# Kernel optimization log

Measured on AMD Instinct MI355X. Metric: run time of the kernel, lower is better.

## Reference

```python
import jax, jax.numpy as jnp
import numpy as np

D_MODEL, N_LEVELS, N_HEADS, N_POINTS = 256, 4, 8, 4
SHAPES = [(100, 100), (50, 50), (25, 25), (13, 13)]  # (H, W) per level


def setup_inputs() -> dict:
    key = jax.random.key(0)
    ks = jax.random.split(key, 8)
    N = 2
    C = D_MODEL
    Len_in = sum(h * w for h, w in SHAPES)
    Lq = Len_in  # encoder self-attention
    query = jax.random.normal(ks[0], (N, Lq, C), jnp.float32)
    reference_points = jax.random.uniform(ks[1], (N, Lq, N_LEVELS, 2), dtype=jnp.float32)
    input_flatten = jax.random.normal(ks[2], (N, Len_in, C), jnp.float32)
    input_spatial_shapes = np.array(SHAPES, dtype=np.int64)
    areas = input_spatial_shapes[:, 0] * input_spatial_shapes[:, 1]
    input_level_start_index = np.concatenate([[0], np.cumsum(areas)[:-1]]).astype(np.int64)
    s = 1.0 / np.sqrt(C)
    Wv = jax.random.uniform(ks[3], (C, C), jnp.float32, -s, s)
    bv = jnp.zeros((C,), jnp.float32)
    # sampling_offsets: small random weight + the module's grid bias init
    Woff = jax.random.normal(ks[4], (N_HEADS * N_LEVELS * N_POINTS * 2, C), jnp.float32) * 0.01
    thetas = jnp.arange(N_HEADS, dtype=jnp.float32) * (2.0 * np.pi / N_HEADS)
    grid = jnp.stack([jnp.cos(thetas), jnp.sin(thetas)], -1)  # (M,2)
    grid = grid / jnp.max(jnp.abs(grid), axis=-1, keepdims=True)
    grid = jnp.tile(grid[:, None, None, :], (1, N_LEVELS, N_POINTS, 1))
    grid = grid * (jnp.arange(N_POINTS, dtype=jnp.float32) + 1.0)[None, None, :, None]
    boff = grid.reshape(-1)
    Wa = jax.random.normal(ks[5], (N_HEADS * N_LEVELS * N_POINTS, C), jnp.float32) * 0.02
    ba = jnp.zeros((N_HEADS * N_LEVELS * N_POINTS,), jnp.float32)
    Wo = jax.random.uniform(ks[6], (C, C), jnp.float32, -s, s)
    bo = jnp.zeros((C,), jnp.float32)
    return {
        'query': query, 'reference_points': reference_points, 'input_flatten': input_flatten,
        'input_spatial_shapes': input_spatial_shapes, 'input_level_start_index': input_level_start_index,
        'Wv': Wv, 'bv': bv, 'Woff': Woff, 'boff': boff, 'Wa': Wa, 'ba': ba, 'Wo': Wo, 'bo': bo,
    }


def _msda_forward(query, reference_points, input_flatten, shapes, starts,
                  Wv, bv, Woff, boff, Wa, ba, Wo, bo):
    N, Lq, C = query.shape
    M, L, P = N_HEADS, N_LEVELS, N_POINTS
    D = C // M
    value = (input_flatten @ Wv.T + bv).reshape(N, -1, M, D)  # (N, Len_in, M, D)
    off = (query @ Woff.T + boff).reshape(N, Lq, M, L, P, 2)
    attn = jax.nn.softmax((query @ Wa.T + ba).reshape(N, Lq, M, L * P), axis=-1)
    attn = attn.reshape(N, Lq, M, L, P)
    # offset_normalizer = (W_l, H_l)
    norm = jnp.asarray(shapes[:, ::-1].copy(), jnp.float32)  # (L, 2)
    loc = reference_points[:, :, None, :, None, :] + off / norm[None, None, None, :, None, :]
    grids = 2.0 * loc - 1.0  # (N, Lq, M, L, P, 2), grid_sample convention
    out = jnp.zeros((N, Lq, M, D), query.dtype)
    for l in range(L):
        H, W = int(shapes[l, 0]), int(shapes[l, 1])
        s0 = int(starts[l])
        v = value[:, s0:s0 + H * W]  # (N, H*W, M, D)
        # align_corners=False unnormalization
        gx = ((grids[:, :, :, l, :, 0] + 1.0) * W - 1.0) / 2.0  # (N, Lq, M, P)
        gy = ((grids[:, :, :, l, :, 1] + 1.0) * H - 1.0) / 2.0
        x0 = jnp.floor(gx); y0 = jnp.floor(gy)
        fx = gx - x0;       fy = gy - y0
        x0i = x0.astype(jnp.int32); y0i = y0.astype(jnp.int32)

        def gather(iy, ix):
            valid = (iy >= 0) & (iy < H) & (ix >= 0) & (ix < W)
            lin = jnp.clip(iy, 0, H - 1) * W + jnp.clip(ix, 0, W - 1)  # (N, Lq, M, P)
            lin2 = lin.transpose(0, 1, 3, 2).reshape(N, Lq * P, M)
            g = jnp.take_along_axis(v, lin2[..., None], axis=1)  # (N, Lq*P, M, D)
            g = g.reshape(N, Lq, P, M, D).transpose(0, 1, 3, 2, 4)  # (N, Lq, M, P, D)
            return g * valid[..., None]  # zero padding outside

        s00 = gather(y0i, x0i)
        s01 = gather(y0i, x0i + 1)
        s10 = gather(y0i + 1, x0i)
        s11 = gather(y0i + 1, x0i + 1)
        sampled = (s00 * ((1 - fy) * (1 - fx))[..., None] + s01 * ((1 - fy) * fx)[..., None]
                   + s10 * (fy * (1 - fx))[..., None] + s11 * (fy * fx)[..., None])
        out = out + jnp.einsum('nqmp,nqmpd->nqmd', attn[:, :, :, l], sampled)
    out = out.reshape(N, Lq, C)
    return out @ Wo.T + bo


def reference(query, reference_points, input_flatten, input_spatial_shapes, input_level_start_index,
              Wv, bv, Woff, boff, Wa, ba, Wo, bo):
    shapes = np.asarray(input_spatial_shapes)
    starts = np.asarray(input_level_start_index)
    return _msda_forward(query, reference_points, input_flatten, shapes, starts,
                         Wv, bv, Woff, boff, Wa, ba, Wo, bo)
```

## Files before the change

kernel.cpp:

```cpp
#include <hip/hip_runtime.h>
#include <math.h>

#define NB   2
#define LQ   13294
#define NROWS (NB*LQ)
#define CDIM 256

typedef unsigned short u16;
typedef unsigned int   u32;
typedef short bf16x8 __attribute__((ext_vector_type(8)));
typedef float f32x4  __attribute__((ext_vector_type(4)));

struct alignas(8) U16x4 { u16 x, y, z, w; };

__device__ __forceinline__ u16 f2bf(float f) {
    u32 u = __builtin_bit_cast(u32, f);
    u += 0x7FFFu + ((u >> 16) & 1u);
    return (u16)(u >> 16);
}
__device__ __forceinline__ float bf2f(u16 h) {
    u32 u = ((u32)h) << 16;
    return __builtin_bit_cast(float, u);
}

__device__ __forceinline__ void gload_lds16(const void* g, void* l) {
    __builtin_amdgcn_global_load_lds(
        (__attribute__((address_space(1))) void*)g,
        (__attribute__((address_space(3))) void*)l, 16, 0, 0);
}

__global__ __launch_bounds__(256)
void prep_all(const float4* __restrict__ query, const float4* __restrict__ inflat,
              const float* __restrict__ Wv, const float* __restrict__ Woff,
              const float* __restrict__ Wa, const float* __restrict__ Wo,
              const float* __restrict__ boff, const float* __restrict__ ba,
              u16* __restrict__ qb, u16* __restrict__ ib,
              u16* __restrict__ wb, float* __restrict__ biascat) {
    const int b = blockIdx.x;
    const int t = threadIdx.x;
    if (b < 6647) {
        int i = b * 256 + t;
        float4 v = query[i];
        U16x4 o{f2bf(v.x), f2bf(v.y), f2bf(v.z), f2bf(v.w)};
        *(U16x4*)&qb[(size_t)i * 4] = o;
    } else if (b < 13294) {
        int i = (b - 6647) * 256 + t;
        float4 v = inflat[i];
        U16x4 o{f2bf(v.x), f2bf(v.y), f2bf(v.z), f2bf(v.w)};
        *(U16x4*)&ib[(size_t)i * 4] = o;
    } else {
        int i = (b - 13294) * 256 + t;
        float v;
        if      (i <  65536) v = Wv[i];
        else if (i < 131072) v = Woff[i - 65536];
        else if (i < 163840) v = Wa[i - 131072];
        else                 v = Wo[i - 163840];
        wb[i] = f2bf(v);
        if (b == 13294) {
            biascat[t] = boff[t];
            if (t < 128) biascat[256 + t] = ba[t];
        }
    }
}

__device__ __forceinline__ void gemm_core128(
    const u16* __restrict__ A, const u16* __restrict__ Bw, int M, int row0,
    u16* As, u16* Bs, f32x4 (&acc)[4][4]) {
    const int tid  = threadIdx.x;
    const int lane = tid & 63;
    const int wave = tid >> 6;
    const int ln16 = lane & 15;
    const int kq   = lane >> 4;
    const int wr   = (wave >> 1) * 64;
    const int wc   = (wave & 1) * 64;

    #pragma unroll
    for (int kt = 0; kt < 4; ++kt) {
        const int k0 = kt * 64;
        #pragma unroll
        for (int it = 0; it < 4; ++it) {
            int chunk = it * 256 + tid;
            int row = chunk >> 3;
            int ch  = chunk & 7;
            int chs = (ch ^ (row & 7)) * 8;
            int gra = min(row0 + row, M - 1);
            gload_lds16(A  + (size_t)gra * 256 + k0 + chs, As + chunk * 8);
            gload_lds16(Bw + (size_t)row * 256 + k0 + chs, Bs + chunk * 8);
        }
        __syncthreads();
        #pragma unroll
        for (int kf = 0; kf < 2; ++kf) {
            const int ck = kf * 4 + kq;
            bf16x8 a[4], b[4];
            #pragma unroll
            for (int i = 0; i < 4; ++i) {
                int r = wr + i * 16 + ln16;
                a[i] = *(const bf16x8*)&As[r * 64 + ((ck ^ (r & 7)) * 8)];
                int c = wc + i * 16 + ln16;
                b[i] = *(const bf16x8*)&Bs[c * 64 + ((ck ^ (c & 7)) * 8)];
            }
            #pragma unroll
            for (int i = 0; i < 4; ++i)
                #pragma unroll
                for (int j = 0; j < 4; ++j)
                    acc[i][j] = __builtin_amdgcn_mfma_f32_16x16x32_bf16(
                        a[i], b[j], acc[i][j], 0, 0, 0);
        }
        __syncthreads();
    }
}

__global__ __launch_bounds__(256, 3)
void gemm_front(const u16* __restrict__ qb, const u16* __restrict__ ib,
                const u16* __restrict__ wb, const float* __restrict__ bv,
                const float* __restrict__ bcat, u16* __restrict__ value,
                float* __restrict__ offb, float* __restrict__ logit, int M) {
    __shared__ u16 As[128 * 64];
    __shared__ u16 Bs[128 * 64];
    const int s    = blockIdx.x;
    const int row0 = blockIdx.y * 128;
    const u16* A  = (s < 2) ? ib : qb;
    const u16* Bw = wb + (size_t)s * 32768;
    const float* bias = (s < 2) ? bv + s * 128 : bcat + (s - 2) * 128;

    f32x4 acc[4][4] = {};
    gemm_core128(A, Bw, M, row0, As, Bs, acc);

    const int lane = threadIdx.x & 63;
    const int wave = threadIdx.x >> 6;
    const int ln16 = lane & 15, kq = lane >> 4;
    const int wr = (wave >> 1) * 64, wc = (wave & 1) * 64;
    #pragma unroll
    for (int j = 0; j < 4; ++j) {
        int lc = wc + j * 16 + ln16;
        float bj = bias[lc];
        #pragma unroll
        for (int i = 0; i < 4; ++i) {
            #pragma unroll
            for (int r = 0; r < 4; ++r) {
                int gr = row0 + wr + i * 16 + kq * 4 + r;
                if (gr < M) {
                    float o = acc[i][j][r] + bj;
                    if (s < 2)
                        value[(size_t)gr * 256 + s * 128 + lc] = f2bf(o);
                    else if (s < 4)
                        offb[(size_t)gr * 256 + (s - 2) * 128 + lc] = o;
                    else
                        logit[(size_t)gr * 128 + lc] = o;
                }
            }
        }
    }
}

__global__ __launch_bounds__(256, 3)
void gemm_out(const u16* __restrict__ A, const u16* __restrict__ Bw0,
              const float* __restrict__ bias, float* __restrict__ C, int M) {
    __shared__ u16 As[128 * 64];
    __shared__ u16 Bs[128 * 64];
    const int s    = blockIdx.x;
    const int row0 = blockIdx.y * 128;
    const u16* Bw = Bw0 + (size_t)s * 32768;

    f32x4 acc[4][4] = {};
    gemm_core128(A, Bw, M, row0, As, Bs, acc);

    const int lane = threadIdx.x & 63;
    const int wave = threadIdx.x >> 6;
    const int ln16 = lane & 15, kq = lane >> 4;
    const int wr = (wave >> 1) * 64, wc = (wave & 1) * 64;
    #pragma unroll
    for (int j = 0; j < 4; ++j) {
        int gc = s * 128 + wc + j * 16 + ln16;
        float bj = bias[gc];
        #pragma unroll
        for (int i = 0; i < 4; ++i) {
            #pragma unroll
            for (int r = 0; r < 4; ++r) {
                int gr = row0 + wr + i * 16 + kq * 4 + r;
                if (gr < M) C[(size_t)gr * 256 + gc] = acc[i][j][r] + bj;
            }
        }
    }
}

__global__ __launch_bounds__(256)
void msda_sample(const u16* __restrict__ value,
                 const float* __restrict__ refpts,
                 const float* __restrict__ off,
                 const float* __restrict__ logits,
                 u16* __restrict__ tmp) {
    __shared__ float sAw[4][8][16];
    __shared__ int   sLin[4][8][17][4];
    __shared__ float sW[4][8][17][4];

    const int t  = threadIdx.x;
    const int qb = blockIdx.x * 4;

    if (t < 32) {
        const int qi = t >> 3, m = t & 7;
        const float* lg = logits + (size_t)(qb + qi) * 128 + m * 16;
        float e[16];
        float mx = -1e30f;
        #pragma unroll
        for (int i = 0; i < 16; ++i) { e[i] = lg[i]; mx = fmaxf(mx, e[i]); }
        float s = 0.f;
        #pragma unroll
        for (int i = 0; i < 16; ++i) { e[i] = __expf(e[i] - mx); s += e[i]; }
        const float inv = 1.f / s;
        #pragma unroll
        for (int i = 0; i < 16; ++i) sAw[qi][m][i] = e[i] * inv;
    }
    __syncthreads();

    #pragma unroll
    for (int j2 = 0; j2 < 2; ++j2) {
        const int job = t + j2 * 256;
        const int qi = job >> 7;
        const int m  = (job >> 4) & 7;
        const int p  = job & 15;
        const int l  = p >> 2, pp = p & 3;
        const int q  = qb + qi;
        const int n  = (q >= LQ) ? 1 : 0;

        const int W = (l == 0) ? 100 : (l == 1) ? 50 : (l == 2) ? 25 : 13;
        const int H = W;
        const int st = (l == 0) ? 0 : (l == 1) ? 10000 : (l == 2) ? 12500 : 13125;

        const float rx = refpts[(size_t)q * 8 + l * 2 + 0];
        const float ry = refpts[(size_t)q * 8 + l * 2 + 1];
        const float ox = off[(size_t)q * 256 + m * 32 + (l * 4 + pp) * 2 + 0];
        const float oy = off[(size_t)q * 256 + m * 32 + (l * 4 + pp) * 2 + 1];

        const float locx = rx + ox / (float)W;
        const float locy = ry + oy / (float)H;
        const float grx = 2.f * locx - 1.f;
        const float gry = 2.f * locy - 1.f;
        const float gx = ((grx + 1.f) * (float)W - 1.f) * 0.5f;
        const float gy = ((gry + 1.f) * (float)H - 1.f) * 0.5f;
        const float x0f = floorf(gx), y0f = floorf(gy);
        const float fx = gx - x0f, fy = gy - y0f;
        const int x0 = (int)x0f, y0 = (int)y0f;
        const int x1 = x0 + 1, y1 = y0 + 1;

        const int cx0 = min(max(x0, 0), W - 1);
        const int cx1 = min(max(x1, 0), W - 1);
        const int cy0 = min(max(y0, 0), H - 1);
        const int cy1 = min(max(y1, 0), H - 1);
        const bool vx0 = (x0 >= 0) & (x0 < W);
        const bool vx1 = (x1 >= 0) & (x1 < W);
        const bool vy0 = (y0 >= 0) & (y0 < H);
        const bool vy1 = (y1 >= 0) & (y1 < H);

        const float aw = sAw[qi][m][p];
        const int base = n * LQ + st;
        sLin[qi][m][p][0] = base + cy0 * W + cx0;
        sLin[qi][m][p][1] = base + cy0 * W + cx1;
        sLin[qi][m][p][2] = base + cy1 * W + cx0;
        sLin[qi][m][p][3] = base + cy1 * W + cx1;
        sW[qi][m][p][0] = (vy0 & vx0) ? aw * (1.f - fy) * (1.f - fx) : 0.f;
        sW[qi][m][p][1] = (vy0 & vx1) ? aw * (1.f - fy) * fx         : 0.f;
        sW[qi][m][p][2] = (vy1 & vx0) ? aw * fy * (1.f - fx)         : 0.f;
        sW[qi][m][p][3] = (vy1 & vx1) ? aw * fy * fx                 : 0.f;
    }
    __syncthreads();

    const int qi = t >> 6;
    const int m  = (t >> 3) & 7;
    const int e  = t & 7;
    const int q  = qb + qi;
    const u16* vch = value + m * 32 + e * 4;

    float ax = 0.f, ay = 0.f, az = 0.f, aw_ = 0.f;
    #pragma unroll
    for (int g = 0; g < 4; ++g) {
        U16x4 raw[16];
        float4 Wt4[4];
        #pragma unroll
        for (int pp = 0; pp < 4; ++pp) {
            int p = g * 4 + pp;
            int4 L = *(const int4*)&sLin[qi][m][p][0];
            Wt4[pp] = *(const float4*)&sW[qi][m][p][0];
            raw[pp * 4 + 0] = *(const U16x4*)(vch + (size_t)L.x * 256);
            raw[pp * 4 + 1] = *(const U16x4*)(vch + (size_t)L.y * 256);
            raw[pp * 4 + 2] = *(const U16x4*)(vch + (size_t)L.z * 256);
            raw[pp * 4 + 3] = *(const U16x4*)(vch + (size_t)L.w * 256);
        }
        #pragma unroll
        for (int pp = 0; pp < 4; ++pp) {
            const float* wp = (const float*)&Wt4[pp];
            #pragma unroll
            for (int c = 0; c < 4; ++c) {
                U16x4 r = raw[pp * 4 + c];
                float wgt = wp[c];
                ax  += wgt * bf2f(r.x);
                ay  += wgt * bf2f(r.y);
                az  += wgt * bf2f(r.z);
                aw_ += wgt * bf2f(r.w);
            }
        }
    }
    U16x4 o{f2bf(ax), f2bf(ay), f2bf(az), f2bf(aw_)};
    *(U16x4*)&tmp[(size_t)q * 256 + m * 32 + e * 4] = o;
}

extern "C" void kernel_launch(void* const* d_in, const int* in_sizes, int n_in,
                              void* d_out, int out_size, void* d_ws, size_t ws_size,
                              hipStream_t stream) {
    const float* query  = (const float*)d_in[0];
    const float* refpts = (const float*)d_in[1];
    const float* inflat = (const float*)d_in[2];
    const float* Wv   = (const float*)d_in[5];
    const float* bv   = (const float*)d_in[6];
    const float* Woff = (const float*)d_in[7];
    const float* boff = (const float*)d_in[8];
    const float* Wa   = (const float*)d_in[9];
    const float* ba   = (const float*)d_in[10];
    const float* Wo   = (const float*)d_in[11];
    const float* bo   = (const float*)d_in[12];
    float* out = (float*)d_out;

    char* ws = (char*)d_ws;
    constexpr size_t SZ16 = (size_t)NROWS * 256 * 2;
    constexpr size_t SZ32 = (size_t)NROWS * 256 * 4;
    constexpr size_t SZL  = (size_t)NROWS * 128 * 4;
    u16*   qb    = (u16*)(ws);
    u16*   ib    = (u16*)(ws + SZ16);
    u16*   value = (u16*)(ws + 2 * SZ16);
    float* offb  = (float*)(ws + 3 * SZ16);
    float* logit = (float*)(ws + 3 * SZ16 + SZ32);
    u16*   wb    = (u16*)(ws + 3 * SZ16 + SZ32 + SZL);
    float* bcat  = (float*)(ws + 3 * SZ16 + SZ32 + SZL + 229376 * 2);
    u16*   tmp   = qb;

    const int RG = (NROWS + 127) / 128;

    hipLaunchKernelGGL(prep_all, dim3(14190), dim3(256), 0, stream,
                       (const float4*)query, (const float4*)inflat,
                       Wv, Woff, Wa, Wo, boff, ba, qb, ib, wb, bcat);

    gemm_front<<<dim3(5, RG), dim3(256), 0, stream>>>(
        qb, ib, wb, bv, bcat, value, offb, logit, NROWS);

    hipLaunchKernelGGL(msda_sample, dim3(NROWS / 4), dim3(256), 0, stream,
                       value, refpts, offb, logit, tmp);

    gemm_out<<<dim3(2, RG), dim3(256), 0, stream>>>(
        tmp, wb + 163840, bo, out, NROWS);
}
```

Before: 232.5 us.

## Fuse fp32-to-bf16 conversion into GEMM loads and vectorize MSDA gather

Removes the separate prep kernel that converted query, input and weights to bf16. The GEMMs now read fp32 directly, convert in registers with packed cvt instructions and store to swizzled LDS. This drops one launch and a bf16 round-trip through memory, at the cost of losing the async global-to-LDS loads for the A operand. The sampling kernel is also reworked: each thread gathers 16-byte chunks over half the points using packed f32x2 FMAs, then combines the two halves with a lane shuffle, and the division by W becomes a multiply by its reciprocal.

```diff
diff --git a/kernel.cpp b/kernel.cpp
--- a/kernel.cpp
+++ b/kernel.cpp
@@ -10,6 +10,7 @@
 typedef unsigned int   u32;
 typedef short bf16x8 __attribute__((ext_vector_type(8)));
 typedef float f32x4  __attribute__((ext_vector_type(4)));
+typedef float f32x2  __attribute__((ext_vector_type(2)));
 
 struct alignas(8) U16x4 { u16 x, y, z, w; };
 
@@ -23,48 +24,27 @@
     return __builtin_bit_cast(float, u);
 }
 
+__device__ __forceinline__ u32 cvtpk(float a, float b) {
+    u32 d;
+    asm("v_cvt_pk_bf16_f32 %0, %1, %2" : "=v"(d) : "v"(a), "v"(b));
+    return d;
+}
+
 __device__ __forceinline__ void gload_lds16(const void* g, void* l) {
     __builtin_amdgcn_global_load_lds(
         (__attribute__((address_space(1))) void*)g,
         (__attribute__((address_space(3))) void*)l, 16, 0, 0);
 }
 
-__global__ __launch_bounds__(256)
-void prep_all(const float4* __restrict__ query, const float4* __restrict__ inflat,
-              const float* __restrict__ Wv, const float* __restrict__ Woff,
-              const float* __restrict__ Wa, const float* __restrict__ Wo,
-              const float* __restrict__ boff, const float* __restrict__ ba,
-              u16* __restrict__ qb, u16* __restrict__ ib,
-              u16* __restrict__ wb, float* __restrict__ biascat) {
-    const int b = blockIdx.x;
-    const int t = threadIdx.x;
-    if (b < 6647) {
-        int i = b * 256 + t;
-        float4 v = query[i];
-        U16x4 o{f2bf(v.x), f2bf(v.y), f2bf(v.z), f2bf(v.w)};
-        *(U16x4*)&qb[(size_t)i * 4] = o;
-    } else if (b < 13294) {
-        int i = (b - 6647) * 256 + t;
-        float4 v = inflat[i];
-        U16x4 o{f2bf(v.x), f2bf(v.y), f2bf(v.z), f2bf(v.w)};
-        *(U16x4*)&ib[(size_t)i * 4] = o;
-    } else {
-        int i = (b - 13294) * 256 + t;
-        float v;
-        if      (i <  65536) v = Wv[i];
-        else if (i < 131072) v = Woff[i - 65536];
-        else if (i < 163840) v = Wa[i - 131072];
-        else                 v = Wo[i - 163840];
-        wb[i] = f2bf(v);
-        if (b == 13294) {
-            biascat[t] = boff[t];
-            if (t < 128) biascat[256 + t] = ba[t];
-        }
-    }
-}
-
-__device__ __forceinline__ void gemm_core128(
-    const u16* __restrict__ A, const u16* __restrict__ Bw, int M, int row0,
+__device__ __forceinline__ f32x2 bfpair(u32 u) {
+    union { u32 w[2]; f32x2 v; } x;
+    x.w[0] = u << 16;
+    x.w[1] = u & 0xFFFF0000u;
+    return x.v;
+}
+
+__device__ __forceinline__ void core_f32src(
+    const float* __restrict__ A, const float* __restrict__ Bf, int M, int row0,
     u16* As, u16* Bs, f32x4 (&acc)[4][4]) {
     const int tid  = threadIdx.x;
     const int lane = tid & 63;
@@ -82,10 +62,22 @@
             int chunk = it * 256 + tid;
             int row = chunk >> 3;
             int ch  = chunk & 7;
-            int chs = (ch ^ (row & 7)) * 8;
+            int dst = row * 64 + ((ch ^ (row & 7)) * 8);
             int gra = min(row0 + row, M - 1);
-            gload_lds16(A  + (size_t)gra * 256 + k0 + chs, As + chunk * 8);
-            gload_lds16(Bw + (size_t)row * 256 + k0 + chs, Bs + chunk * 8);
+            const float* pa = A + (size_t)gra * 256 + k0 + ch * 8;
+            float4 a0 = *(const float4*)pa;
+            float4 a1 = *(const float4*)(pa + 4);
+            uint4 ua;
+            ua.x = cvtpk(a0.x, a0.y); ua.y = cvtpk(a0.z, a0.w);
+            ua.z = cvtpk(a1.x, a1.y); ua.w = cvtpk(a1.z, a1.w);
+            *(uint4*)&As[dst] = ua;
+            const float* pb = Bf + (size_t)row * 256 + k0 + ch * 8;
+            float4 b0 = *(const float4*)pb;
+            float4 b1 = *(const float4*)(pb + 4);
+            uint4 ub;
+            ub.x = cvtpk(b0.x, b0.y); ub.y = cvtpk(b0.z, b0.w);
+            ub.z = cvtpk(b1.x, b1.y); ub.w = cvtpk(b1.z, b1.w);
+            *(uint4*)&Bs[dst] = ub;
         }
         __syncthreads();
         #pragma unroll
@@ -110,21 +102,82 @@
     }
 }
 
+__device__ __forceinline__ void core_mixed(
+    const u16* __restrict__ A, const float* __restrict__ Bf, int M, int row0,
+    u16* As, u16* Bs, f32x4 (&acc)[4][4]) {
+    const int tid  = threadIdx.x;
+    const int lane = tid & 63;
+    const int wave = tid >> 6;
+    const int ln16 = lane & 15;
+    const int kq   = lane >> 4;
+    const int wr   = (wave >> 1) * 64;
+    const int wc   = (wave & 1) * 64;
+
+    #pragma unroll
+    for (int kt = 0; kt < 4; ++kt) {
+        const int k0 = kt * 64;
+        #pragma unroll
+        for (int it = 0; it < 4; ++it) {
+            int chunk = it * 256 + tid;
+            int row = chunk >> 3;
+            int ch  = chunk & 7;
+            int chs = (ch ^ (row & 7)) * 8;
+            int gra = min(row0 + row, M - 1);
+            gload_lds16(A + (size_t)gra * 256 + k0 + chs, As + chunk * 8);
+            const float* pb = Bf + (size_t)row * 256 + k0 + ch * 8;
+            float4 b0 = *(const float4*)pb;
+            float4 b1 = *(const float4*)(pb + 4);
+            uint4 ub;
+            ub.x = cvtpk(b0.x, b0.y); ub.y = cvtpk(b0.z, b0.w);
+            ub.z = cvtpk(b1.x, b1.y); ub.w = cvtpk(b1.z, b1.w);
+            *(uint4*)&Bs[row * 64 + chs] = ub;
+        }
+        __syncthreads();
+        #pragma unroll
+        for (int kf = 0; kf < 2; ++kf) {
+            const int ck = kf * 4 + kq;
+            bf16x8 a[4], b[4];
+            #pragma unroll
+            for (int i = 0; i < 4; ++i) {
+                int r = wr + i * 16 + ln16;
+                a[i] = *(const bf16x8*)&As[r * 64 + ((ck ^ (r & 7)) * 8)];
+                int c = wc + i * 16 + ln16;
+                b[i] = *(const bf16x8*)&Bs[c * 64 + ((ck ^ (c & 7)) * 8)];
+            }
+            #pragma unroll
+            for (int i = 0; i < 4; ++i)
+                #pragma unroll
+                for (int j = 0; j < 4; ++j)
+                    acc[i][j] = __builtin_amdgcn_mfma_f32_16x16x32_bf16(
+                        a[i], b[j], acc[i][j], 0, 0, 0);
+        }
+        __syncthreads();
+    }
+}
+
 __global__ __launch_bounds__(256, 3)
-void gemm_front(const u16* __restrict__ qb, const u16* __restrict__ ib,
-                const u16* __restrict__ wb, const float* __restrict__ bv,
-                const float* __restrict__ bcat, u16* __restrict__ value,
-                float* __restrict__ offb, float* __restrict__ logit, int M) {
+void gemm_front(const float* __restrict__ query, const float* __restrict__ inflat,
+                const float* __restrict__ Wv, const float* __restrict__ Woff,
+                const float* __restrict__ Wa, const float* __restrict__ bv,
+                const float* __restrict__ boff, const float* __restrict__ ba,
+                u16* __restrict__ value, float* __restrict__ offb,
+                float* __restrict__ logit, int M) {
     __shared__ u16 As[128 * 64];
     __shared__ u16 Bs[128 * 64];
     const int s    = blockIdx.x;
     const int row0 = blockIdx.y * 128;
-    const u16* A  = (s < 2) ? ib : qb;
-    const u16* Bw = wb + (size_t)s * 32768;
-    const float* bias = (s < 2) ? bv + s * 128 : bcat + (s - 2) * 128;
+    const float* A  = (s < 2) ? inflat : query;
+    const float* Bf = (s == 0) ? Wv
+                    : (s == 1) ? Wv + 32768
+                    : (s == 2) ? Woff
+                    : (s == 3) ? Woff + 32768
+                    : Wa;
+    const float* bias = (s < 2) ? bv + s * 128
+                      : (s < 4) ? boff + (s - 2) * 128
+                      : ba;
 
     f32x4 acc[4][4] = {};
-    gemm_core128(A, Bw, M, row0, As, Bs, acc);
+    core_f32src(A, Bf, M, row0, As, Bs, acc);
 
     const int lane = threadIdx.x & 63;
     const int wave = threadIdx.x >> 6;
@@ -154,16 +207,16 @@
 }
 
 __global__ __launch_bounds__(256, 3)
-void gemm_out(const u16* __restrict__ A, const u16* __restrict__ Bw0,
+void gemm_out(const u16* __restrict__ A, const float* __restrict__ Wo,
               const float* __restrict__ bias, float* __restrict__ C, int M) {
     __shared__ u16 As[128 * 64];
     __shared__ u16 Bs[128 * 64];
     const int s    = blockIdx.x;
     const int row0 = blockIdx.y * 128;
-    const u16* Bw = Bw0 + (size_t)s * 32768;
+    const float* Bf = Wo + (size_t)s * 32768;
 
     f32x4 acc[4][4] = {};
-    gemm_core128(A, Bw, M, row0, As, Bs, acc);
+    core_mixed(A, Bf, M, row0, As, Bs, acc);
 
     const int lane = threadIdx.x & 63;
     const int wave = threadIdx.x >> 6;
@@ -226,14 +279,16 @@
         const int W = (l == 0) ? 100 : (l == 1) ? 50 : (l == 2) ? 25 : 13;
         const int H = W;
         const int st = (l == 0) ? 0 : (l == 1) ? 10000 : (l == 2) ? 12500 : 13125;
+        const float invW = (l == 0) ? 0.01f : (l == 1) ? 0.02f
+                         : (l == 2) ? 0.04f : (1.f / 13.f);
 
         const float rx = refpts[(size_t)q * 8 + l * 2 + 0];
         const float ry = refpts[(size_t)q * 8 + l * 2 + 1];
         const float ox = off[(size_t)q * 256 + m * 32 + (l * 4 + pp) * 2 + 0];
         const float oy = off[(size_t)q * 256 + m * 32 + (l * 4 + pp) * 2 + 1];
 
-        const float locx = rx + ox / (float)W;
-        const float locy = ry + oy / (float)H;
+        const float locx = rx + ox * invW;
+        const float locy = ry + oy * invW;
         const float grx = 2.f * locx - 1.f;
         const float gry = 2.f * locy - 1.f;
         const float gx = ((grx + 1.f) * (float)W - 1.f) * 0.5f;
@@ -267,41 +322,56 @@
 
     const int qi = t >> 6;
     const int m  = (t >> 3) & 7;
-    const int e  = t & 7;
+    const int hf = (t >> 2) & 1;
+    const int e4 = t & 3;
     const int q  = qb + qi;
-    const u16* vch = value + m * 32 + e * 4;
-
-    float ax = 0.f, ay = 0.f, az = 0.f, aw_ = 0.f;
-    #pragma unroll
-    for (int g = 0; g < 4; ++g) {
-        U16x4 raw[16];
-        float4 Wt4[4];
-        #pragma unroll
-        for (int pp = 0; pp < 4; ++pp) {
-            int p = g * 4 + pp;
-            int4 L = *(const int4*)&sLin[qi][m][p][0];
-            Wt4[pp] = *(const float4*)&sW[qi][m][p][0];
-            raw[pp * 4 + 0] = *(const U16x4*)(vch + (size_t)L.x * 256);
-            raw[pp * 4 + 1] = *(const U16x4*)(vch + (size_t)L.y * 256);
-            raw[pp * 4 + 2] = *(const U16x4*)(vch + (size_t)L.z * 256);
-            raw[pp * 4 + 3] = *(const U16x4*)(vch + (size_t)L.w * 256);
-        }
-        #pragma unroll
-        for (int pp = 0; pp < 4; ++pp) {
-            const float* wp = (const float*)&Wt4[pp];
-            #pragma unroll
-            for (int c = 0; c < 4; ++c) {
-                U16x4 r = raw[pp * 4 + c];
-                float wgt = wp[c];
-                ax  += wgt * bf2f(r.x);
-                ay  += wgt * bf2f(r.y);
-                az  += wgt * bf2f(r.z);
-                aw_ += wgt * bf2f(r.w);
-            }
-        }
-    }
-    U16x4 o{f2bf(ax), f2bf(ay), f2bf(az), f2bf(aw_)};
-    *(U16x4*)&tmp[(size_t)q * 256 + m * 32 + e * 4] = o;
+    const char* vb = (const char*)value;
+    const u32 choff = (u32)(m * 64 + e4 * 16);
+
+    f32x2 a2[4] = {{0.f, 0.f}, {0.f, 0.f}, {0.f, 0.f}, {0.f, 0.f}};
+    #pragma unroll
+    for (int pp = 0; pp < 8; ++pp) {
+        const int p = hf * 8 + pp;
+        int4   L  = *(const int4*)  &sLin[qi][m][p][0];
+        float4 Wt = *(const float4*)&sW  [qi][m][p][0];
+        uint4 r0 = *(const uint4*)(vb + ((u32)L.x * 512u + choff));
+        uint4 r1 = *(const uint4*)(vb + ((u32)L.y * 512u + choff));
+        uint4 r2 = *(const uint4*)(vb + ((u32)L.z * 512u + choff));
+        uint4 r3 = *(const uint4*)(vb + ((u32)L.w * 512u + choff));
+        {
+            f32x2 w2 = {Wt.x, Wt.x};
+            a2[0] += w2 * bfpair(r0.x); a2[1] += w2 * bfpair(r0.y);
+            a2[2] += w2 * bfpair(r0.z); a2[3] += w2 * bfpair(r0.w);
+        }
+        {
+            f32x2 w2 = {Wt.y, Wt.y};
+            a2[0] += w2 * bfpair(r1.x); a2[1] += w2 * bfpair(r1.y);
+            a2[2] += w2 * bfpair(r1.z); a2[3] += w2 * bfpair(r1.w);
+        }
+        {
+            f32x2 w2 = {Wt.z, Wt.z};
+            a2[0] += w2 * bfpair(r2.x); a2[1] += w2 * bfpair(r2.y);
+            a2[2] += w2 * bfpair(r2.z); a2[3] += w2 * bfpair(r2.w);
+        }
+        {
+            f32x2 w2 = {Wt.w, Wt.w};
+            a2[0] += w2 * bfpair(r3.x); a2[1] += w2 * bfpair(r3.y);
+            a2[2] += w2 * bfpair(r3.z); a2[3] += w2 * bfpair(r3.w);
+        }
+    }
+    #pragma unroll
+    for (int k = 0; k < 4; ++k) {
+        a2[k].x += __shfl_xor(a2[k].x, 4);
+        a2[k].y += __shfl_xor(a2[k].y, 4);
+    }
+    if (hf == 0) {
+        uint4 o;
+        o.x = (u32)f2bf(a2[0].x) | ((u32)f2bf(a2[0].y) << 16);
+        o.y = (u32)f2bf(a2[1].x) | ((u32)f2bf(a2[1].y) << 16);
+        o.z = (u32)f2bf(a2[2].x) | ((u32)f2bf(a2[2].y) << 16);
+        o.w = (u32)f2bf(a2[3].x) | ((u32)f2bf(a2[3].y) << 16);
+        *(uint4*)((char*)tmp + ((u32)q * 512u + choff)) = o;
+    }
 }
 
 extern "C" void kernel_launch(void* const* d_in, const int* in_sizes, int n_in,
@@ -323,28 +393,19 @@
     char* ws = (char*)d_ws;
     constexpr size_t SZ16 = (size_t)NROWS * 256 * 2;
     constexpr size_t SZ32 = (size_t)NROWS * 256 * 4;
-    constexpr size_t SZL  = (size_t)NROWS * 128 * 4;
-    u16*   qb    = (u16*)(ws);
-    u16*   ib    = (u16*)(ws + SZ16);
+    u16*   tmp   = (u16*)(ws);
     u16*   value = (u16*)(ws + 2 * SZ16);
     float* offb  = (float*)(ws + 3 * SZ16);
     float* logit = (float*)(ws + 3 * SZ16 + SZ32);
-    u16*   wb    = (u16*)(ws + 3 * SZ16 + SZ32 + SZL);
-    float* bcat  = (float*)(ws + 3 * SZ16 + SZ32 + SZL + 229376 * 2);
-    u16*   tmp   = qb;
 
     const int RG = (NROWS + 127) / 128;
 
-    hipLaunchKernelGGL(prep_all, dim3(14190), dim3(256), 0, stream,
-                       (const float4*)query, (const float4*)inflat,
-                       Wv, Woff, Wa, Wo, boff, ba, qb, ib, wb, bcat);
-
     gemm_front<<<dim3(5, RG), dim3(256), 0, stream>>>(
-        qb, ib, wb, bv, bcat, value, offb, logit, NROWS);
+        query, inflat, Wv, Woff, Wa, bv, boff, ba, value, offb, logit, NROWS);
 
     hipLaunchKernelGGL(msda_sample, dim3(NROWS / 4), dim3(256), 0, stream,
                        value, refpts, offb, logit, tmp);
 
     gemm_out<<<dim3(2, RG), dim3(256), 0, stream>>>(
-        tmp, wb + 163840, bo, out, NROWS);
-}
+        tmp, Wo, bo, out, NROWS);
+}
```

Measured after the change: 240.6 us. 3.5% more time.
